# Kernel tuning notes

Hardware: AMD Instinct MI355X
Metric: run time of the kernel (lower is better)

## Reference

```python
import jax, jax.numpy as jnp
import numpy as np

BATCH, N_IN, N_OUT, DEGREE = 128, 2048, 1024, 15
EPSILON = 1.0
TEMPERATURE = 0.1
NEG_FILL = -1000000000.0


def setup_inputs() -> dict:
    key = jax.random.key(0)
    k1, k2, k3 = jax.random.split(key, 3)
    x = jax.random.normal(k1, (BATCH, N_IN), dtype=jnp.float32)
    weights = jax.random.normal(k2, (N_OUT, N_IN), dtype=jnp.float32) * 0.02
    # buffer: (rand(n_out, n_in) < degree/n_in).float()
    synaptic_mask = (jax.random.uniform(k3, (N_OUT, N_IN)) < DEGREE / N_IN).astype(jnp.float32)
    return {"x": x, "weights": weights, "synaptic_mask": synaptic_mask}


def reference(x, weights, synaptic_mask):
    n_in = x.shape[1]
    # torch.median returns the LOWER of the two middle values for even n:
    # sorted index (n-1)//2
    consensus = jnp.sort(x, axis=1)[:, (n_in - 1) // 2][:, None]  # [B, 1]
    gate = (jnp.abs(x - consensus) < EPSILON).astype(x.dtype)      # [B, n_in]
    gated_x = x * gate                                             # [B, n_in]
    # dense broadcast-add: [B, n_out, n_in]
    combined = gated_x[:, None, :] + weights[None, :, :]
    masked_z = jnp.where(synaptic_mask == 0.0, NEG_FILL, combined)
    return TEMPERATURE * jax.nn.logsumexp(masked_z / TEMPERATURE, axis=2)  # [B, n_out]
```

## Files before the change

### kernel.cpp

```cpp
#include <hip/hip_runtime.h>
#include <math.h>

#define BATCH 128
#define N_IN 2048
#define N_OUT 1024
#define MAXK 40
#define BCAP 64
#define TEMP 0.1f
#define INV_TEMP 10.0f
#define NEG_FILL -1.0e9f
#define WLO -0.1875f
#define WHI 0.1875f
#define BINSCALE 682.6666666f

__device__ __forceinline__ unsigned int f2key(float f) {
    unsigned int b = __float_as_uint(f);
    return (b & 0x80000000u) ? ~b : (b | 0x80000000u);
}
__device__ __forceinline__ float key2f(unsigned int u) {
    unsigned int b = (u & 0x80000000u) ? (u & 0x7FFFFFFFu) : ~u;
    return __uint_as_float(b);
}

__global__ __launch_bounds__(256) void k_prep(const float* __restrict__ x,
                                              const float* __restrict__ w,
                                              const float* __restrict__ msk,
                                              int* __restrict__ cnt,
                                              int2* __restrict__ listsT,
                                              float* __restrict__ med) {
    __shared__ unsigned int hist[256];
    __shared__ unsigned int wsum4[4];
    __shared__ unsigned int sel[2];
    __shared__ float sbin[BCAP];
    __shared__ int s_nb;
    __shared__ float s_med;
    __shared__ int sidx[2][MAXK];

    const int tid = threadIdx.x;
    const int lane = tid & 63;
    const int wwid = tid >> 6;
    const int bid = (int)blockIdx.x;

    if (bid < BATCH) {
        const int b = bid;
        const float4* xr = (const float4*)(x + (size_t)b * N_IN);
        float4 va = xr[tid], vb = xr[tid + 256];
        float vals[8] = {va.x, va.y, va.z, va.w, vb.x, vb.y, vb.z, vb.w};

        hist[tid] = 0;
        if (tid == 0) s_nb = 0;
        __syncthreads();

        int cb = 0;
#pragma unroll
        for (int j = 0; j < 8; ++j) {
            float v = vals[j];
            cb += (v < WLO) ? 1 : 0;
            if (v >= WLO && v < WHI) {
                int bin = (int)((v - WLO) * BINSCALE);
                bin = (bin > 255) ? 255 : bin;
                atomicAdd(&hist[bin], 1u);
            }
        }
        int sb = cb;
#pragma unroll
        for (int off = 1; off < 64; off <<= 1) sb += __shfl_xor(sb, off, 64);
        if (lane == 0) wsum4[wwid] = (unsigned int)sb;
        __syncthreads();
        const int c_lo = (int)(wsum4[0] + wsum4[1] + wsum4[2] + wsum4[3]);
        const int R = (N_IN - 1) / 2 - c_lo;

        unsigned int hv = hist[tid];
        unsigned int sv = hv;
#pragma unroll
        for (int off = 1; off < 64; off <<= 1) {
            unsigned int t = __shfl_up(sv, off, 64);
            if (lane >= off) sv += t;
        }
        __syncthreads();
        if (lane == 63) wsum4[wwid] = sv;
        if (tid == 0) sel[0] = 0xFFFFFFFFu;
        __syncthreads();
        unsigned int base = 0;
        for (int ww = 0; ww < wwid; ++ww) base += wsum4[ww];
        const unsigned int incl = sv + base;
        const unsigned int excl = incl - hv;
        const int n_c = (int)(wsum4[0] + wsum4[1] + wsum4[2] + wsum4[3]);
        if (R >= 0 && R < n_c && (unsigned int)R >= excl && (unsigned int)R < incl) {
            sel[0] = (unsigned int)tid;
            sel[1] = (unsigned int)R - excl;
        }
        __syncthreads();

        bool fast_ok = (R >= 0 && R < n_c && sel[0] != 0xFFFFFFFFu);
        if (fast_ok) {
            const int B = (int)sel[0];
            const int r2 = (int)sel[1];
#pragma unroll
            for (int j = 0; j < 8; ++j) {
                float v = vals[j];
                if (v >= WLO && v < WHI) {
                    int bin = (int)((v - WLO) * BINSCALE);
                    bin = (bin > 255) ? 255 : bin;
                    if (bin == B) {
                        int p = atomicAdd(&s_nb, 1);
                        if (p < BCAP) sbin[p] = v;
                    }
                }
            }
            __syncthreads();
            const int nb = s_nb;
            if (nb <= BCAP) {
                if (tid < nb) {
                    float v = sbin[tid];
                    int nlt = 0, neq = 0;
                    for (int j = 0; j < nb; ++j) {
                        float u = sbin[j];
                        nlt += (u < v) ? 1 : 0;
                        neq += (u == v) ? 1 : 0;
                    }
                    if (nlt <= r2 && r2 < nlt + neq) s_med = v;
                }
            } else {
                fast_ok = false;
            }
            __syncthreads();
        }
        if (!fast_ok) {
            unsigned int prefix = 0;
            unsigned int k = (N_IN - 1) / 2;
            for (int pos = 24; pos >= 0; pos -= 8) {
                hist[tid] = 0;
                __syncthreads();
                const unsigned int hmask = (pos == 24) ? 0u : (0xFFFFFFFFu << (pos + 8));
#pragma unroll
                for (int j = 0; j < 8; ++j) {
                    unsigned int u = f2key(vals[j]);
                    if ((u & hmask) == (prefix & hmask))
                        atomicAdd(&hist[(u >> pos) & 0xFFu], 1u);
                }
                __syncthreads();
                unsigned int v = hist[tid];
                unsigned int s2 = v;
#pragma unroll
                for (int off = 1; off < 64; off <<= 1) {
                    unsigned int t = __shfl_up(s2, off, 64);
                    if (lane >= off) s2 += t;
                }
                if (lane == 63) wsum4[wwid] = s2;
                __syncthreads();
                unsigned int bs = 0;
                for (int ww = 0; ww < wwid; ++ww) bs += wsum4[ww];
                const unsigned int inc2 = s2 + bs;
                const unsigned int exc2 = inc2 - v;
                if (k >= exc2 && k < inc2) {
                    sel[0] = (unsigned int)tid;
                    sel[1] = k - exc2;
                }
                __syncthreads();
                prefix |= sel[0] << pos;
                k = sel[1];
                __syncthreads();
            }
            if (tid == 0) s_med = key2f(prefix);
            __syncthreads();
        }
        if (tid == 0) med[bid] = s_med;
    } else {
        const int o0 = (bid - BATCH) * 2;
        const float4* m0 = (const float4*)(msk + (size_t)o0 * N_IN);
        const float4* m1 = (const float4*)(msk + (size_t)(o0 + 1) * N_IN);
        float4 m0a = m0[tid], m0b = m0[tid + 256];
        float4 m1a = m1[tid], m1b = m1[tid + 256];
        float mv0[8] = {m0a.x, m0a.y, m0a.z, m0a.w, m0b.x, m0b.y, m0b.z, m0b.w};
        float mv1[8] = {m1a.x, m1a.y, m1a.z, m1a.w, m1b.x, m1b.y, m1b.z, m1b.w};

        int c0 = 0, c1 = 0;
#pragma unroll
        for (int j = 0; j < 8; ++j) {
            c0 += (mv0[j] != 0.0f) ? 1 : 0;
            c1 += (mv1[j] != 0.0f) ? 1 : 0;
        }
        int packed = (c0 << 16) | c1;
        int sv = packed;
#pragma unroll
        for (int off = 1; off < 64; off <<= 1) {
            int t = __shfl_up(sv, off, 64);
            if (lane >= off) sv += t;
        }
        if (lane == 63) wsum4[wwid] = (unsigned int)sv;
        __syncthreads();
        int base = 0;
        for (int ww = 0; ww < wwid; ++ww) base += (int)wsum4[ww];
        const int excl = base + sv - packed;
        const int tot = (int)(wsum4[0] + wsum4[1] + wsum4[2] + wsum4[3]);
        const int ct0 = tot >> 16;
        const int ct1 = tot & 0xFFFF;
        if (tid == 0) {
            cnt[o0] = ct0;
            cnt[o0 + 1] = ct1;
        }

        int p0 = (excl >> 16) & 0xFFFF;
        int p1 = excl & 0xFFFF;
#pragma unroll
        for (int j = 0; j < 8; ++j) {
            const int idx = (j < 4) ? 4 * tid + j : 1024 + 4 * tid + (j - 4);
            if (mv0[j] != 0.0f) {
                if (p0 < MAXK) sidx[0][p0] = idx;
                ++p0;
            }
            if (mv1[j] != 0.0f) {
                if (p1 < MAXK) sidx[1][p1] = idx;
                ++p1;
            }
        }
        __syncthreads();

        const int cc0 = (ct0 < MAXK) ? ct0 : MAXK;
        const int cc1 = (ct1 < MAXK) ? ct1 : MAXK;
        if (tid < cc0) {
            const int idx = sidx[0][tid];
            listsT[tid * N_OUT + o0] = make_int2(idx, __float_as_int(w[(size_t)o0 * N_IN + idx]));
        } else if (tid >= 64 && tid - 64 < cc1) {
            const int idx = sidx[1][tid - 64];
            listsT[(tid - 64) * N_OUT + (o0 + 1)] =
                make_int2(idx, __float_as_int(w[(size_t)(o0 + 1) * N_IN + idx]));
        }
    }
}

__global__ __launch_bounds__(512) void k_lse(const float* __restrict__ x,
                                             const float* __restrict__ medv,
                                             const int* __restrict__ cnt,
                                             const int2* __restrict__ listsT,
                                             const float* __restrict__ w,
                                             const float* __restrict__ msk,
                                             float* __restrict__ out) {
    __shared__ float sgx[N_IN];
    const int b = blockIdx.x >> 1;
    const int h = blockIdx.x & 1;
    const int tid = threadIdx.x;

    const float med = medv[b];
    const float4* xr = (const float4*)(x + (size_t)b * N_IN);
    float4 va = xr[tid];
    float4 ga;
    ga.x = (fabsf(va.x - med) < 1.0f) ? va.x : 0.0f;
    ga.y = (fabsf(va.y - med) < 1.0f) ? va.y : 0.0f;
    ga.z = (fabsf(va.z - med) < 1.0f) ? va.z : 0.0f;
    ga.w = (fabsf(va.w - med) < 1.0f) ? va.w : 0.0f;
    ((float4*)sgx)[tid] = ga;
    __syncthreads();

    const int o = h * 512 + tid;
    const int c = cnt[o];
    float res;
    if (c == 0) {
        res = NEG_FILL;
    } else if (c <= MAXK) {
        int2 e = listsT[o];
        float m = (sgx[e.x] + __int_as_float(e.y)) * INV_TEMP;
        float s = 1.0f;
        for (int j = 1; j < c; ++j) {
            e = listsT[j * N_OUT + o];
            float v = (sgx[e.x] + __int_as_float(e.y)) * INV_TEMP;
            float mn = fmaxf(m, v);
            s = s * __expf(m - mn) + __expf(v - mn);
            m = mn;
        }
        res = TEMP * (m + __logf(s));
    } else {
        const float* mr = msk + (size_t)o * N_IN;
        const float* wr = w + (size_t)o * N_IN;
        float m = -INFINITY, s = 0.0f;
        for (int i = 0; i < N_IN; ++i) {
            if (mr[i] != 0.0f) {
                float v = (sgx[i] + wr[i]) * INV_TEMP;
                float mn = fmaxf(m, v);
                s = s * __expf(m - mn) + __expf(v - mn);
                m = mn;
            }
        }
        res = TEMP * (m + __logf(s));
    }
    out[(size_t)b * N_OUT + o] = res;
}

extern "C" void kernel_launch(void* const* d_in, const int* in_sizes, int n_in,
                              void* d_out, int out_size, void* d_ws, size_t ws_size,
                              hipStream_t stream) {
    const float* x = (const float*)d_in[0];
    const float* w = (const float*)d_in[1];
    const float* msk = (const float*)d_in[2];
    float* out = (float*)d_out;

    int* cnt = (int*)d_ws;
    int2* listsT = (int2*)(cnt + N_OUT);
    float* med = (float*)(listsT + (size_t)MAXK * N_OUT);

    hipLaunchKernelGGL(k_prep, dim3(BATCH + N_OUT / 2), dim3(256), 0, stream,
                       x, w, msk, cnt, listsT, med);
    hipLaunchKernelGGL(k_lse, dim3(BATCH * 2), dim3(512), 0, stream,
                       x, med, cnt, listsT, w, msk, out);
}
```

Measured before the change: 16.09 us.

## Fuse median selection into LSE kernel, separate mask compaction kernel

Median computation moves out of the prep kernel and into the logsumexp kernel. Each of the two blocks per batch row now computes the median redundantly with 512 threads, each holding 4 values. This removes the global round trip for the median and makes the first kernel purely mask compaction. The cost is duplicated median work per row and a longer second kernel. The second kernel still depends on the compaction output.

```diff
diff --git a/kernel.cpp b/kernel.cpp
--- a/kernel.cpp
+++ b/kernel.cpp
@@ -22,234 +22,241 @@
     return __uint_as_float(b);
 }
 
-__global__ __launch_bounds__(256) void k_prep(const float* __restrict__ x,
+__global__ __launch_bounds__(256) void k_compact(const float* __restrict__ w,
+                                                 const float* __restrict__ msk,
+                                                 int* __restrict__ cnt,
+                                                 int2* __restrict__ listsT) {
+    __shared__ unsigned int wscr[4];
+    __shared__ int sidx[2][MAXK];
+
+    const int tid = threadIdx.x;
+    const int lane = tid & 63;
+    const int wvid = tid >> 6;
+    const int o0 = (int)blockIdx.x * 2;
+
+    const float4* m0 = (const float4*)(msk + (size_t)o0 * N_IN);
+    const float4* m1 = (const float4*)(msk + (size_t)(o0 + 1) * N_IN);
+    float4 m0a = m0[tid], m0b = m0[tid + 256];
+    float4 m1a = m1[tid], m1b = m1[tid + 256];
+    float mv0[8] = {m0a.x, m0a.y, m0a.z, m0a.w, m0b.x, m0b.y, m0b.z, m0b.w};
+    float mv1[8] = {m1a.x, m1a.y, m1a.z, m1a.w, m1b.x, m1b.y, m1b.z, m1b.w};
+
+    int c0 = 0, c1 = 0;
+#pragma unroll
+    for (int j = 0; j < 8; ++j) {
+        c0 += (mv0[j] != 0.0f) ? 1 : 0;
+        c1 += (mv1[j] != 0.0f) ? 1 : 0;
+    }
+    int packed = (c0 << 16) | c1;
+    int sv = packed;
+#pragma unroll
+    for (int off = 1; off < 64; off <<= 1) {
+        int t = __shfl_up(sv, off, 64);
+        if (lane >= off) sv += t;
+    }
+    if (lane == 63) wscr[wvid] = (unsigned int)sv;
+    __syncthreads();
+    int base = 0;
+    for (int ww = 0; ww < wvid; ++ww) base += (int)wscr[ww];
+    const int excl = base + sv - packed;
+    const int tot = (int)(wscr[0] + wscr[1] + wscr[2] + wscr[3]);
+    const int ct0 = tot >> 16;
+    const int ct1 = tot & 0xFFFF;
+    if (tid == 0) {
+        cnt[o0] = ct0;
+        cnt[o0 + 1] = ct1;
+    }
+
+    int p0 = (excl >> 16) & 0xFFFF;
+    int p1 = excl & 0xFFFF;
+#pragma unroll
+    for (int j = 0; j < 8; ++j) {
+        const int idx = (j < 4) ? 4 * tid + j : 1024 + 4 * tid + (j - 4);
+        if (mv0[j] != 0.0f) {
+            if (p0 < MAXK) sidx[0][p0] = idx;
+            ++p0;
+        }
+        if (mv1[j] != 0.0f) {
+            if (p1 < MAXK) sidx[1][p1] = idx;
+            ++p1;
+        }
+    }
+    __syncthreads();
+
+    const int cc0 = (ct0 < MAXK) ? ct0 : MAXK;
+    const int cc1 = (ct1 < MAXK) ? ct1 : MAXK;
+    if (tid < cc0) {
+        const int idx = sidx[0][tid];
+        listsT[tid * N_OUT + o0] = make_int2(idx, __float_as_int(w[(size_t)o0 * N_IN + idx]));
+    } else if (tid >= 64 && tid - 64 < cc1) {
+        const int idx = sidx[1][tid - 64];
+        listsT[(tid - 64) * N_OUT + (o0 + 1)] =
+            make_int2(idx, __float_as_int(w[(size_t)(o0 + 1) * N_IN + idx]));
+    }
+}
+
+__global__ __launch_bounds__(512) void k_mlse(const float* __restrict__ x,
+                                              const int* __restrict__ cnt,
+                                              const int2* __restrict__ listsT,
                                               const float* __restrict__ w,
                                               const float* __restrict__ msk,
-                                              int* __restrict__ cnt,
-                                              int2* __restrict__ listsT,
-                                              float* __restrict__ med) {
+                                              float* __restrict__ out) {
+    __shared__ float sgx[N_IN];
     __shared__ unsigned int hist[256];
-    __shared__ unsigned int wsum4[4];
+    __shared__ unsigned int wscr[8];
     __shared__ unsigned int sel[2];
     __shared__ float sbin[BCAP];
     __shared__ int s_nb;
     __shared__ float s_med;
-    __shared__ int sidx[2][MAXK];
-
+
+    const int b = (int)blockIdx.x >> 1;
+    const int h = (int)blockIdx.x & 1;
     const int tid = threadIdx.x;
     const int lane = tid & 63;
-    const int wwid = tid >> 6;
-    const int bid = (int)blockIdx.x;
-
-    if (bid < BATCH) {
-        const int b = bid;
-        const float4* xr = (const float4*)(x + (size_t)b * N_IN);
-        float4 va = xr[tid], vb = xr[tid + 256];
-        float vals[8] = {va.x, va.y, va.z, va.w, vb.x, vb.y, vb.z, vb.w};
-
-        hist[tid] = 0;
-        if (tid == 0) s_nb = 0;
-        __syncthreads();
-
-        int cb = 0;
-#pragma unroll
-        for (int j = 0; j < 8; ++j) {
+    const int wvid = tid >> 6;
+
+    const float4* xr = (const float4*)(x + (size_t)b * N_IN);
+    float4 va = xr[tid];
+    float vals[4] = {va.x, va.y, va.z, va.w};
+
+    if (tid < 256) hist[tid] = 0;
+    if (tid == 0) s_nb = 0;
+    __syncthreads();
+
+    int cb = 0;
+#pragma unroll
+    for (int j = 0; j < 4; ++j) {
+        float v = vals[j];
+        cb += (v < WLO) ? 1 : 0;
+        if (v >= WLO && v < WHI) {
+            int bin = (int)((v - WLO) * BINSCALE);
+            bin = (bin > 255) ? 255 : bin;
+            atomicAdd(&hist[bin], 1u);
+        }
+    }
+    int sb = cb;
+#pragma unroll
+    for (int off = 1; off < 64; off <<= 1) sb += __shfl_xor(sb, off, 64);
+    if (lane == 0) wscr[wvid] = (unsigned int)sb;
+    __syncthreads();
+    int c_lo = 0;
+#pragma unroll
+    for (int ww = 0; ww < 8; ++ww) c_lo += (int)wscr[ww];
+    const int R = (N_IN - 1) / 2 - c_lo;
+    __syncthreads();
+
+    unsigned int hv = 0, sv = 0;
+    if (tid < 256) {
+        hv = hist[tid];
+        sv = hv;
+#pragma unroll
+        for (int off = 1; off < 64; off <<= 1) {
+            unsigned int t = __shfl_up(sv, off, 64);
+            if (lane >= off) sv += t;
+        }
+        if (lane == 63) wscr[wvid] = sv;
+    }
+    if (tid == 0) sel[0] = 0xFFFFFFFFu;
+    __syncthreads();
+    const int n_c = (int)(wscr[0] + wscr[1] + wscr[2] + wscr[3]);
+    if (tid < 256) {
+        unsigned int base = 0;
+        for (int ww = 0; ww < wvid; ++ww) base += wscr[ww];
+        const unsigned int incl = sv + base;
+        const unsigned int excl = incl - hv;
+        if (R >= 0 && R < n_c && (unsigned int)R >= excl && (unsigned int)R < incl) {
+            sel[0] = (unsigned int)tid;
+            sel[1] = (unsigned int)R - excl;
+        }
+    }
+    __syncthreads();
+
+    bool fast_ok = (R >= 0 && R < n_c && sel[0] != 0xFFFFFFFFu);
+    if (fast_ok) {
+        const int B = (int)sel[0];
+        const int r2 = (int)sel[1];
+#pragma unroll
+        for (int j = 0; j < 4; ++j) {
             float v = vals[j];
-            cb += (v < WLO) ? 1 : 0;
             if (v >= WLO && v < WHI) {
                 int bin = (int)((v - WLO) * BINSCALE);
                 bin = (bin > 255) ? 255 : bin;
-                atomicAdd(&hist[bin], 1u);
-            }
-        }
-        int sb = cb;
-#pragma unroll
-        for (int off = 1; off < 64; off <<= 1) sb += __shfl_xor(sb, off, 64);
-        if (lane == 0) wsum4[wwid] = (unsigned int)sb;
+                if (bin == B) {
+                    int p = atomicAdd(&s_nb, 1);
+                    if (p < BCAP) sbin[p] = v;
+                }
+            }
+        }
         __syncthreads();
-        const int c_lo = (int)(wsum4[0] + wsum4[1] + wsum4[2] + wsum4[3]);
-        const int R = (N_IN - 1) / 2 - c_lo;
-
-        unsigned int hv = hist[tid];
-        unsigned int sv = hv;
-#pragma unroll
-        for (int off = 1; off < 64; off <<= 1) {
-            unsigned int t = __shfl_up(sv, off, 64);
-            if (lane >= off) sv += t;
+        const int nb = s_nb;
+        if (nb <= BCAP) {
+            if (tid < nb) {
+                float v = sbin[tid];
+                int nlt = 0, neq = 0;
+                for (int j = 0; j < nb; ++j) {
+                    float u = sbin[j];
+                    nlt += (u < v) ? 1 : 0;
+                    neq += (u == v) ? 1 : 0;
+                }
+                if (nlt <= r2 && r2 < nlt + neq) s_med = v;
+            }
+        } else {
+            fast_ok = false;
         }
         __syncthreads();
-        if (lane == 63) wsum4[wwid] = sv;
-        if (tid == 0) sel[0] = 0xFFFFFFFFu;
-        __syncthreads();
-        unsigned int base = 0;
-        for (int ww = 0; ww < wwid; ++ww) base += wsum4[ww];
-        const unsigned int incl = sv + base;
-        const unsigned int excl = incl - hv;
-        const int n_c = (int)(wsum4[0] + wsum4[1] + wsum4[2] + wsum4[3]);
-        if (R >= 0 && R < n_c && (unsigned int)R >= excl && (unsigned int)R < incl) {
-            sel[0] = (unsigned int)tid;
-            sel[1] = (unsigned int)R - excl;
-        }
-        __syncthreads();
-
-        bool fast_ok = (R >= 0 && R < n_c && sel[0] != 0xFFFFFFFFu);
-        if (fast_ok) {
-            const int B = (int)sel[0];
-            const int r2 = (int)sel[1];
-#pragma unroll
-            for (int j = 0; j < 8; ++j) {
-                float v = vals[j];
-                if (v >= WLO && v < WHI) {
-                    int bin = (int)((v - WLO) * BINSCALE);
-                    bin = (bin > 255) ? 255 : bin;
-                    if (bin == B) {
-                        int p = atomicAdd(&s_nb, 1);
-                        if (p < BCAP) sbin[p] = v;
-                    }
-                }
-            }
-            __syncthreads();
-            const int nb = s_nb;
-            if (nb <= BCAP) {
-                if (tid < nb) {
-                    float v = sbin[tid];
-                    int nlt = 0, neq = 0;
-                    for (int j = 0; j < nb; ++j) {
-                        float u = sbin[j];
-                        nlt += (u < v) ? 1 : 0;
-                        neq += (u == v) ? 1 : 0;
-                    }
-                    if (nlt <= r2 && r2 < nlt + neq) s_med = v;
-                }
-            } else {
-                fast_ok = false;
-            }
-            __syncthreads();
-        }
-        if (!fast_ok) {
-            unsigned int prefix = 0;
-            unsigned int k = (N_IN - 1) / 2;
-            for (int pos = 24; pos >= 0; pos -= 8) {
-                hist[tid] = 0;
-                __syncthreads();
-                const unsigned int hmask = (pos == 24) ? 0u : (0xFFFFFFFFu << (pos + 8));
-#pragma unroll
-                for (int j = 0; j < 8; ++j) {
-                    unsigned int u = f2key(vals[j]);
-                    if ((u & hmask) == (prefix & hmask))
-                        atomicAdd(&hist[(u >> pos) & 0xFFu], 1u);
-                }
-                __syncthreads();
-                unsigned int v = hist[tid];
-                unsigned int s2 = v;
+    }
+    if (!fast_ok) {
+        unsigned int prefix = 0;
+        unsigned int k = (N_IN - 1) / 2;
+        for (int pos = 24; pos >= 0; pos -= 8) {
+            if (tid < 256) hist[tid] = 0;
+            __syncthreads();
+            const unsigned int hmask = (pos == 24) ? 0u : (0xFFFFFFFFu << (pos + 8));
+#pragma unroll
+            for (int j = 0; j < 4; ++j) {
+                unsigned int u = f2key(vals[j]);
+                if ((u & hmask) == (prefix & hmask))
+                    atomicAdd(&hist[(u >> pos) & 0xFFu], 1u);
+            }
+            __syncthreads();
+            unsigned int v = 0, s2 = 0;
+            if (tid < 256) {
+                v = hist[tid];
+                s2 = v;
 #pragma unroll
                 for (int off = 1; off < 64; off <<= 1) {
                     unsigned int t = __shfl_up(s2, off, 64);
                     if (lane >= off) s2 += t;
                 }
-                if (lane == 63) wsum4[wwid] = s2;
-                __syncthreads();
+            }
+            __syncthreads();
+            if (tid < 256 && lane == 63) wscr[wvid] = s2;
+            __syncthreads();
+            if (tid < 256) {
                 unsigned int bs = 0;
-                for (int ww = 0; ww < wwid; ++ww) bs += wsum4[ww];
+                for (int ww = 0; ww < wvid; ++ww) bs += wscr[ww];
                 const unsigned int inc2 = s2 + bs;
                 const unsigned int exc2 = inc2 - v;
                 if (k >= exc2 && k < inc2) {
                     sel[0] = (unsigned int)tid;
                     sel[1] = k - exc2;
                 }
-                __syncthreads();
-                prefix |= sel[0] << pos;
-                k = sel[1];
-                __syncthreads();
-            }
-            if (tid == 0) s_med = key2f(prefix);
-            __syncthreads();
-        }
-        if (tid == 0) med[bid] = s_med;
-    } else {
-        const int o0 = (bid - BATCH) * 2;
-        const float4* m0 = (const float4*)(msk + (size_t)o0 * N_IN);
-        const float4* m1 = (const float4*)(msk + (size_t)(o0 + 1) * N_IN);
-        float4 m0a = m0[tid], m0b = m0[tid + 256];
-        float4 m1a = m1[tid], m1b = m1[tid + 256];
-        float mv0[8] = {m0a.x, m0a.y, m0a.z, m0a.w, m0b.x, m0b.y, m0b.z, m0b.w};
-        float mv1[8] = {m1a.x, m1a.y, m1a.z, m1a.w, m1b.x, m1b.y, m1b.z, m1b.w};
-
-        int c0 = 0, c1 = 0;
-#pragma unroll
-        for (int j = 0; j < 8; ++j) {
-            c0 += (mv0[j] != 0.0f) ? 1 : 0;
-            c1 += (mv1[j] != 0.0f) ? 1 : 0;
-        }
-        int packed = (c0 << 16) | c1;
-        int sv = packed;
-#pragma unroll
-        for (int off = 1; off < 64; off <<= 1) {
-            int t = __shfl_up(sv, off, 64);
-            if (lane >= off) sv += t;
-        }
-        if (lane == 63) wsum4[wwid] = (unsigned int)sv;
+            }
+            __syncthreads();
+            prefix |= sel[0] << pos;
+            k = sel[1];
+            __syncthreads();
+        }
+        if (tid == 0) s_med = key2f(prefix);
         __syncthreads();
-        int base = 0;
-        for (int ww = 0; ww < wwid; ++ww) base += (int)wsum4[ww];
-        const int excl = base + sv - packed;
-        const int tot = (int)(wsum4[0] + wsum4[1] + wsum4[2] + wsum4[3]);
-        const int ct0 = tot >> 16;
-        const int ct1 = tot & 0xFFFF;
-        if (tid == 0) {
-            cnt[o0] = ct0;
-            cnt[o0 + 1] = ct1;
-        }
-
-        int p0 = (excl >> 16) & 0xFFFF;
-        int p1 = excl & 0xFFFF;
-#pragma unroll
-        for (int j = 0; j < 8; ++j) {
-            const int idx = (j < 4) ? 4 * tid + j : 1024 + 4 * tid + (j - 4);
-            if (mv0[j] != 0.0f) {
-                if (p0 < MAXK) sidx[0][p0] = idx;
-                ++p0;
-            }
-            if (mv1[j] != 0.0f) {
-                if (p1 < MAXK) sidx[1][p1] = idx;
-                ++p1;
-            }
-        }
-        __syncthreads();
-
-        const int cc0 = (ct0 < MAXK) ? ct0 : MAXK;
-        const int cc1 = (ct1 < MAXK) ? ct1 : MAXK;
-        if (tid < cc0) {
-            const int idx = sidx[0][tid];
-            listsT[tid * N_OUT + o0] = make_int2(idx, __float_as_int(w[(size_t)o0 * N_IN + idx]));
-        } else if (tid >= 64 && tid - 64 < cc1) {
-            const int idx = sidx[1][tid - 64];
-            listsT[(tid - 64) * N_OUT + (o0 + 1)] =
-                make_int2(idx, __float_as_int(w[(size_t)(o0 + 1) * N_IN + idx]));
-        }
-    }
-}
-
-__global__ __launch_bounds__(512) void k_lse(const float* __restrict__ x,
-                                             const float* __restrict__ medv,
-                                             const int* __restrict__ cnt,
-                                             const int2* __restrict__ listsT,
-                                             const float* __restrict__ w,
-                                             const float* __restrict__ msk,
-                                             float* __restrict__ out) {
-    __shared__ float sgx[N_IN];
-    const int b = blockIdx.x >> 1;
-    const int h = blockIdx.x & 1;
-    const int tid = threadIdx.x;
-
-    const float med = medv[b];
-    const float4* xr = (const float4*)(x + (size_t)b * N_IN);
-    float4 va = xr[tid];
+    }
+    const float med = s_med;
+
     float4 ga;
-    ga.x = (fabsf(va.x - med) < 1.0f) ? va.x : 0.0f;
-    ga.y = (fabsf(va.y - med) < 1.0f) ? va.y : 0.0f;
-    ga.z = (fabsf(va.z - med) < 1.0f) ? va.z : 0.0f;
-    ga.w = (fabsf(va.w - med) < 1.0f) ? va.w : 0.0f;
+    ga.x = (fabsf(vals[0] - med) < 1.0f) ? vals[0] : 0.0f;
+    ga.y = (fabsf(vals[1] - med) < 1.0f) ? vals[1] : 0.0f;
+    ga.z = (fabsf(vals[2] - med) < 1.0f) ? vals[2] : 0.0f;
+    ga.w = (fabsf(vals[3] - med) < 1.0f) ? vals[3] : 0.0f;
     ((float4*)sgx)[tid] = ga;
     __syncthreads();
 
@@ -297,10 +304,9 @@
 
     int* cnt = (int*)d_ws;
     int2* listsT = (int2*)(cnt + N_OUT);
-    float* med = (float*)(listsT + (size_t)MAXK * N_OUT);
-
-    hipLaunchKernelGGL(k_prep, dim3(BATCH + N_OUT / 2), dim3(256), 0, stream,
-                       x, w, msk, cnt, listsT, med);
-    hipLaunchKernelGGL(k_lse, dim3(BATCH * 2), dim3(512), 0, stream,
-                       x, med, cnt, listsT, w, msk, out);
-}
+
+    hipLaunchKernelGGL(k_compact, dim3(N_OUT / 2), dim3(256), 0, stream,
+                       w, msk, cnt, listsT);
+    hipLaunchKernelGGL(k_mlse, dim3(BATCH * 2), dim3(512), 0, stream,
+                       x, cnt, listsT, w, msk, out);
+}
```

After: 17.55 us. 9.1% more time.
